# Kernel tuning notes

Measured on AMD Instinct MI355X. Metric: run time of the kernel, lower is better.

Reference implementation:

```python
import jax, jax.numpy as jnp
import numpy as np

DIM = 64  # per-head key dim; temp = sqrt(DIM)
B, S = 32, 2048  # flattened batch*heads, seq_len


def setup_inputs() -> dict:
    key = jax.random.key(0)
    kq, kk, kv = jax.random.split(key, 3)
    q = jax.random.normal(kq, (B, S, DIM), dtype=jnp.float32)
    k = jax.random.normal(kk, (B, S, DIM), dtype=jnp.float32)
    v = jax.random.normal(kv, (B, S, DIM), dtype=jnp.float32)
    return {"q": q, "k": k, "v": v}


def reference(q, k, v):
    temp = np.sqrt(DIM).astype(np.float32)
    # attn = bmm(q, k^T) / sqrt(dim): [B, Sq, Sk]
    attn = jnp.einsum("bqd,bkd->bqk", q, k) / temp
    # softmax over key dim (the view/softmax(dim=1)/view trick == softmax over last axis)
    attn = jax.nn.softmax(attn, axis=-1)
    # dropout p=0.0 -> identity
    out = jnp.einsum("bqk,bkd->bqd", attn, v)
    return out
```

## Files before the change

### kernel.cpp

```cpp
#include <hip/hip_runtime.h>
#include <hip/hip_bf16.h>

#define S_ 2048
#define D_ 64
#define BM 128
#define BN 128
#define KSTR 72
#define VSTR 136
#define KP  260

typedef __attribute__((ext_vector_type(8))) short bf16x8;
typedef __attribute__((ext_vector_type(16))) float f32x16;

__device__ __forceinline__ unsigned int cvtpk(float lo, float hi) {
    unsigned int r;
    asm("v_cvt_pk_bf16_f32 %0, %1, %2" : "=v"(r) : "v"(lo), "v"(hi));
    return r;
}
__device__ __forceinline__ ushort bf16c(float x) {
    return (ushort)(cvtpk(x, x) & 0xffffu);
}

__global__ __launch_bounds__(256) void prep(const float* __restrict__ k,
                                            const float* __restrict__ v,
                                            ushort* __restrict__ kbf,
                                            ushort* __restrict__ vtb) {
    __shared__ ushort Ld[64 * KP];
    const int batch = blockIdx.x >> 3;
    const int w0    = (blockIdx.x & 7) * 256;
    const int t     = threadIdx.x;

    const float* kb = k   + (size_t)batch * S_ * D_ + (size_t)w0 * D_;
    ushort*      ko = kbf + (size_t)batch * S_ * D_ + (size_t)w0 * D_;
#pragma unroll
    for (int p = 0; p < 8; ++p) {
        const int c = p * 256 + t;
        const float4 a = *(const float4*)(kb + c * 8);
        const float4 b = *(const float4*)(kb + c * 8 + 4);
        uint4 o;
        o.x = cvtpk(a.x, a.y); o.y = cvtpk(a.z, a.w);
        o.z = cvtpk(b.x, b.y); o.w = cvtpk(b.z, b.w);
        *(uint4*)(ko + c * 8) = o;
    }

    const float* vb = v + (size_t)batch * S_ * D_ + (size_t)w0 * D_;
#pragma unroll
    for (int i = 0; i < 16; ++i) {
        const int c   = i * 256 + t;
        const int key = c >> 4;
        const int dp  = (c & 15) * 4;
        const float4 a = *(const float4*)(vb + key * 64 + dp);
        Ld[(dp + 0) * KP + key] = bf16c(a.x);
        Ld[(dp + 1) * KP + key] = bf16c(a.y);
        Ld[(dp + 2) * KP + key] = bf16c(a.z);
        Ld[(dp + 3) * KP + key] = bf16c(a.w);
    }
    __syncthreads();

    const int w  = t >> 6;
    const int l  = t & 63;
    ushort* vo = vtb + (size_t)batch * D_ * S_;
#pragma unroll
    for (int j = 0; j < 8; ++j) {
        const int d    = j * 8 + w * 2 + (l >> 5);
        const int keyc = (l & 31) * 8;
        const uint4 val = *(const uint4*)(&Ld[d * KP + keyc]);
        *(uint4*)(vo + (size_t)d * S_ + w0 + keyc) = val;
    }
}

__global__ __launch_bounds__(256, 2) void fattn(const float* __restrict__ q,
                                                const ushort* __restrict__ kbf,
                                                const ushort* __restrict__ vtb_g,
                                                float* __restrict__ out) {
    __shared__ ushort Kt[BN * KSTR];
    __shared__ ushort Vt[D_ * VSTR];

    const int tid  = threadIdx.x;
    const int wid  = tid >> 6;
    const int lane = tid & 63;
    const int lq   = lane & 31;
    const int lh   = lane >> 5;

    const int batch = blockIdx.x >> 4;
    const int qtile = blockIdx.x & 15;

    const float*  qp  = q     + (size_t)batch * S_ * D_;
    const ushort* kp  = kbf   + (size_t)batch * S_ * D_;
    const ushort* vtb = vtb_g + (size_t)batch * D_ * S_;

    const float SC = 0.18033688011112042f;
    const int qrow = qtile * BM + wid * 32 + lq;
    bf16x8 qf[4];
    {
        const float* qr = qp + (size_t)qrow * D_ + 8 * lh;
#pragma unroll
        for (int kk = 0; kk < 4; ++kk) {
            union { bf16x8 v; unsigned int u[4]; } uq;
#pragma unroll
            for (int j = 0; j < 4; ++j)
                uq.u[j] = cvtpk(qr[kk * 16 + 2 * j] * SC, qr[kk * 16 + 2 * j + 1] * SC);
            qf[kk] = uq.v;
        }
    }

    f32x16 O[2];
#pragma unroll
    for (int md = 0; md < 2; ++md)
#pragma unroll
        for (int j = 0; j < 16; ++j) O[md][j] = 0.f;
    float m = -INFINITY, l = 0.f;

    for (int kt = 0; kt < S_; kt += BN) {
        __syncthreads();
        {
            const ushort* ktile = kp + (size_t)kt * D_;
#pragma unroll
            for (int p = 0; p < 4; ++p) {
                const int c = p * 256 + tid;
                *(uint4*)(&Kt[(c >> 3) * KSTR + (c & 7) * 8]) =
                    *(const uint4*)(ktile + c * 8);
            }
#pragma unroll
            for (int p = 0; p < 4; ++p) {
                const int c = p * 256 + tid;
                const int d = c >> 4, part = c & 15;
                *(uint4*)(&Vt[d * VSTR + part * 8]) =
                    *(const uint4*)(vtb + (size_t)d * S_ + kt + part * 8);
            }
        }
        __syncthreads();

        f32x16 sa[4];
#pragma unroll
        for (int mt = 0; mt < 4; ++mt) {
            const ushort* krow = &Kt[(mt * 32 + lq) * KSTR + 8 * lh];
            f32x16 acc;
#pragma unroll
            for (int j = 0; j < 16; ++j) acc[j] = 0.f;
#pragma unroll
            for (int kk = 0; kk < 4; ++kk) {
                const bf16x8 kf = *(const bf16x8*)(krow + kk * 16);
                acc = __builtin_amdgcn_mfma_f32_32x32x16_bf16(kf, qf[kk], acc, 0, 0, 0);
            }
            sa[mt] = acc;
        }

        float tg[4];
#pragma unroll
        for (int g = 0; g < 4; ++g) {
            float a  = fmaxf(sa[g][0], sa[g][1]);
            float b  = fmaxf(sa[g][2], sa[g][3]);
            float c  = fmaxf(sa[g][4], sa[g][5]);
            float d0 = fmaxf(sa[g][6], sa[g][7]);
            float e  = fmaxf(sa[g][8], sa[g][9]);
            float f  = fmaxf(sa[g][10], sa[g][11]);
            float h  = fmaxf(sa[g][12], sa[g][13]);
            float i  = fmaxf(sa[g][14], sa[g][15]);
            a = fmaxf(a, b); c = fmaxf(c, d0); e = fmaxf(e, f); h = fmaxf(h, i);
            tg[g] = fmaxf(fmaxf(a, c), fmaxf(e, h));
        }
        float tm = fmaxf(fmaxf(tg[0], tg[1]), fmaxf(tg[2], tg[3]));
        tm = fmaxf(tm, __shfl_xor(tm, 32, 64));
        const float mnew = fmaxf(m, tm);
        const float alpha = __builtin_amdgcn_exp2f(m - mnew);

        float r0 = 0.f, r1 = 0.f, r2 = 0.f, r3 = 0.f;
#pragma unroll
        for (int g = 0; g < 4; ++g)
#pragma unroll
            for (int j = 0; j < 16; j += 4) {
                const float e0 = __builtin_amdgcn_exp2f(sa[g][j]     - mnew);
                const float e1 = __builtin_amdgcn_exp2f(sa[g][j + 1] - mnew);
                const float e2 = __builtin_amdgcn_exp2f(sa[g][j + 2] - mnew);
                const float e3 = __builtin_amdgcn_exp2f(sa[g][j + 3] - mnew);
                sa[g][j] = e0; sa[g][j + 1] = e1; sa[g][j + 2] = e2; sa[g][j + 3] = e3;
                r0 += e0; r1 += e1; r2 += e2; r3 += e3;
            }
        float rs = (r0 + r1) + (r2 + r3);
        rs += __shfl_xor(rs, 32, 64);
        l = l * alpha + rs;
        m = mnew;
#pragma unroll
        for (int md = 0; md < 2; ++md)
#pragma unroll
            for (int j = 0; j < 16; ++j) O[md][j] *= alpha;

#pragma unroll
        for (int g = 0; g < 4; ++g) {
#pragma unroll
            for (int h = 0; h < 2; ++h) {
                union { bf16x8 v; unsigned int u[4]; } pf;
#pragma unroll
                for (int i = 0; i < 4; ++i)
                    pf.u[i] = cvtpk(sa[g][h * 8 + 2 * i], sa[g][h * 8 + 2 * i + 1]);
                const int koff = g * 32 + h * 16 + 4 * lh;
#pragma unroll
                for (int md = 0; md < 2; ++md) {
                    const ushort* vb = &Vt[(md * 32 + lq) * VSTR + koff];
                    union { bf16x8 v; uint2 p[2]; } vf;
                    vf.p[0] = *(const uint2*)(vb);
                    vf.p[1] = *(const uint2*)(vb + 8);
                    O[md] = __builtin_amdgcn_mfma_f32_32x32x16_bf16(vf.v, pf.v, O[md], 0, 0, 0);
                }
            }
        }
    }

    const float linv = 1.0f / l;
    float* op = out + (size_t)batch * S_ * D_ + (size_t)qrow * D_;
#pragma unroll
    for (int md = 0; md < 2; ++md) {
#pragma unroll
        for (int r4 = 0; r4 < 4; ++r4) {
            const int d = md * 32 + r4 * 8 + 4 * lh;
            float4 st;
            st.x = O[md][r4 * 4 + 0] * linv;
            st.y = O[md][r4 * 4 + 1] * linv;
            st.z = O[md][r4 * 4 + 2] * linv;
            st.w = O[md][r4 * 4 + 3] * linv;
            *(float4*)(op + d) = st;
        }
    }
}

extern "C" void kernel_launch(void* const* d_in, const int* in_sizes, int n_in,
                              void* d_out, int out_size, void* d_ws, size_t ws_size,
                              hipStream_t stream) {
    const float* q = (const float*)d_in[0];
    const float* k = (const float*)d_in[1];
    const float* v = (const float*)d_in[2];
    float* o = (float*)d_out;

    ushort* kbf = (ushort*)d_ws;
    ushort* vtb = kbf + (size_t)32 * S_ * D_;

    prep<<<dim3(256), dim3(256), 0, stream>>>(k, v, kbf, vtb);
    fattn<<<dim3(512), dim3(256), 0, stream>>>(q, kbf, vtb, o);
}
```

Before: 139.8 us.

## Fuse K/V bf16 conversion and V transpose into attention kernel

Removes the separate prep kernel and has the attention kernel load fp32 K and V tiles directly, converting them to bf16 in registers and transposing V through shared memory each iteration. It also remaps block indices so that blocks sharing a batch land on the same XCD, which should improve L2 reuse of K/V. The aim is to save a kernel launch and the workspace round trip. In exchange, every one of the 16 q-tile blocks per batch now redoes the conversion and transpose, reads twice the bytes per K/V tile, and pays an extra shared-memory buffer and barrier per iteration.

```diff
diff --git a/kernel.cpp b/kernel.cpp
--- a/kernel.cpp
+++ b/kernel.cpp
@@ -7,7 +7,6 @@
 #define BN 128
 #define KSTR 72
 #define VSTR 136
-#define KP  260
 
 typedef __attribute__((ext_vector_type(8))) short bf16x8;
 typedef __attribute__((ext_vector_type(16))) float f32x16;
@@ -17,63 +16,13 @@
     asm("v_cvt_pk_bf16_f32 %0, %1, %2" : "=v"(r) : "v"(lo), "v"(hi));
     return r;
 }
-__device__ __forceinline__ ushort bf16c(float x) {
-    return (ushort)(cvtpk(x, x) & 0xffffu);
-}
-
-__global__ __launch_bounds__(256) void prep(const float* __restrict__ k,
-                                            const float* __restrict__ v,
-                                            ushort* __restrict__ kbf,
-                                            ushort* __restrict__ vtb) {
-    __shared__ ushort Ld[64 * KP];
-    const int batch = blockIdx.x >> 3;
-    const int w0    = (blockIdx.x & 7) * 256;
-    const int t     = threadIdx.x;
-
-    const float* kb = k   + (size_t)batch * S_ * D_ + (size_t)w0 * D_;
-    ushort*      ko = kbf + (size_t)batch * S_ * D_ + (size_t)w0 * D_;
-#pragma unroll
-    for (int p = 0; p < 8; ++p) {
-        const int c = p * 256 + t;
-        const float4 a = *(const float4*)(kb + c * 8);
-        const float4 b = *(const float4*)(kb + c * 8 + 4);
-        uint4 o;
-        o.x = cvtpk(a.x, a.y); o.y = cvtpk(a.z, a.w);
-        o.z = cvtpk(b.x, b.y); o.w = cvtpk(b.z, b.w);
-        *(uint4*)(ko + c * 8) = o;
-    }
-
-    const float* vb = v + (size_t)batch * S_ * D_ + (size_t)w0 * D_;
-#pragma unroll
-    for (int i = 0; i < 16; ++i) {
-        const int c   = i * 256 + t;
-        const int key = c >> 4;
-        const int dp  = (c & 15) * 4;
-        const float4 a = *(const float4*)(vb + key * 64 + dp);
-        Ld[(dp + 0) * KP + key] = bf16c(a.x);
-        Ld[(dp + 1) * KP + key] = bf16c(a.y);
-        Ld[(dp + 2) * KP + key] = bf16c(a.z);
-        Ld[(dp + 3) * KP + key] = bf16c(a.w);
-    }
-    __syncthreads();
-
-    const int w  = t >> 6;
-    const int l  = t & 63;
-    ushort* vo = vtb + (size_t)batch * D_ * S_;
-#pragma unroll
-    for (int j = 0; j < 8; ++j) {
-        const int d    = j * 8 + w * 2 + (l >> 5);
-        const int keyc = (l & 31) * 8;
-        const uint4 val = *(const uint4*)(&Ld[d * KP + keyc]);
-        *(uint4*)(vo + (size_t)d * S_ + w0 + keyc) = val;
-    }
-}
 
 __global__ __launch_bounds__(256, 2) void fattn(const float* __restrict__ q,
-                                                const ushort* __restrict__ kbf,
-                                                const ushort* __restrict__ vtb_g,
+                                                const float* __restrict__ kg,
+                                                const float* __restrict__ vg,
                                                 float* __restrict__ out) {
     __shared__ ushort Kt[BN * KSTR];
+    __shared__ ushort Vs[BN * KSTR];
     __shared__ ushort Vt[D_ * VSTR];
 
     const int tid  = threadIdx.x;
@@ -82,12 +31,15 @@
     const int lq   = lane & 31;
     const int lh   = lane >> 5;
 
-    const int batch = blockIdx.x >> 4;
-    const int qtile = blockIdx.x & 15;
-
-    const float*  qp  = q     + (size_t)batch * S_ * D_;
-    const ushort* kp  = kbf   + (size_t)batch * S_ * D_;
-    const ushort* vtb = vtb_g + (size_t)batch * D_ * S_;
+    const int bid   = blockIdx.x;
+    const int xcd   = bid & 7;
+    const int slot  = bid >> 3;
+    const int batch = xcd + 8 * (slot >> 4);
+    const int qtile = slot & 15;
+
+    const float* qp = q  + (size_t)batch * S_ * D_;
+    const float* kp = kg + (size_t)batch * S_ * D_;
+    const float* vp = vg + (size_t)batch * S_ * D_;
 
     const float SC = 0.18033688011112042f;
     const int qrow = qtile * BM + wid * 32 + lq;
@@ -114,19 +66,23 @@
     for (int kt = 0; kt < S_; kt += BN) {
         __syncthreads();
         {
-            const ushort* ktile = kp + (size_t)kt * D_;
+            const float* ksrc = kp + (size_t)kt * D_;
+            const float* vsrc = vp + (size_t)kt * D_;
 #pragma unroll
             for (int p = 0; p < 4; ++p) {
                 const int c = p * 256 + tid;
-                *(uint4*)(&Kt[(c >> 3) * KSTR + (c & 7) * 8]) =
-                    *(const uint4*)(ktile + c * 8);
-            }
-#pragma unroll
-            for (int p = 0; p < 4; ++p) {
-                const int c = p * 256 + tid;
-                const int d = c >> 4, part = c & 15;
-                *(uint4*)(&Vt[d * VSTR + part * 8]) =
-                    *(const uint4*)(vtb + (size_t)d * S_ + kt + part * 8);
+                const float4 a  = *(const float4*)(ksrc + c * 8);
+                const float4 b  = *(const float4*)(ksrc + c * 8 + 4);
+                uint4 ok;
+                ok.x = cvtpk(a.x, a.y); ok.y = cvtpk(a.z, a.w);
+                ok.z = cvtpk(b.x, b.y); ok.w = cvtpk(b.z, b.w);
+                *(uint4*)(&Kt[(c >> 3) * KSTR + (c & 7) * 8]) = ok;
+                const float4 va = *(const float4*)(vsrc + c * 8);
+                const float4 vb = *(const float4*)(vsrc + c * 8 + 4);
+                uint4 ov;
+                ov.x = cvtpk(va.x, va.y); ov.y = cvtpk(va.z, va.w);
+                ov.z = cvtpk(vb.x, vb.y); ov.w = cvtpk(vb.z, vb.w);
+                *(uint4*)(&Vs[(c >> 3) * KSTR + (c & 7) * 8]) = ov;
             }
         }
         __syncthreads();
@@ -144,6 +100,23 @@
                 acc = __builtin_amdgcn_mfma_f32_32x32x16_bf16(kf, qf[kk], acc, 0, 0, 0);
             }
             sa[mt] = acc;
+        }
+
+        {
+            const int d = tid & 63;
+#pragma unroll
+            for (int j = 0; j < 4; ++j) {
+                const int chunk = (tid >> 6) + 4 * j;
+                const ushort* src = &Vs[(chunk * 8) * KSTR + d];
+                const unsigned int x0 = src[0 * KSTR], x1 = src[1 * KSTR];
+                const unsigned int x2 = src[2 * KSTR], x3 = src[3 * KSTR];
+                const unsigned int x4 = src[4 * KSTR], x5 = src[5 * KSTR];
+                const unsigned int x6 = src[6 * KSTR], x7 = src[7 * KSTR];
+                uint4 o;
+                o.x = x0 | (x1 << 16); o.y = x2 | (x3 << 16);
+                o.z = x4 | (x5 << 16); o.w = x6 | (x7 << 16);
+                *(uint4*)(&Vt[d * VSTR + chunk * 8]) = o;
+            }
         }
 
         float tg[4];
@@ -186,6 +159,8 @@
 #pragma unroll
             for (int j = 0; j < 16; ++j) O[md][j] *= alpha;
 
+        __syncthreads();
+
 #pragma unroll
         for (int g = 0; g < 4; ++g) {
 #pragma unroll
@@ -232,9 +207,5 @@
     const float* v = (const float*)d_in[2];
     float* o = (float*)d_out;
 
-    ushort* kbf = (ushort*)d_ws;
-    ushort* vtb = kbf + (size_t)32 * S_ * D_;
-
-    prep<<<dim3(256), dim3(256), 0, stream>>>(k, v, kbf, vtb);
-    fattn<<<dim3(512), dim3(256), 0, stream>>>(q, kbf, vtb, o);
+    fattn<<<dim3(512), dim3(256), 0, stream>>>(q, k, v, o);
 }
```

Measured after the change: 137.5 us. No clear change (-1.7%).
